# Kernel optimization log

Hardware: AMD Instinct MI355X
Metric: run time of the kernel (lower is better)

The kernel has to match this reference:

```python
import jax, jax.numpy as jnp
import numpy as np

RADIUS = 1.5
NUM_BASES = 128
HIDDEN = 256
B = 512        # molecules
N_ATOMS = 64   # atoms per molecule
BOX = 4.0      # box side -> density 1 atom/unit^3, avg degree ~8 at r=1.5
V = B * N_ATOMS
E_FIXED = 262144


def setup_inputs() -> dict:
    key = jax.random.key(0)
    kp, kx, kw1, kw2 = jax.random.split(key, 4)
    # positions, grouped per molecule so the radius graph respects batch_index
    pos = np.asarray(jax.random.uniform(kp, (B, N_ATOMS, 3), dtype=jnp.float32)) * BOX
    diff = pos[:, :, None, :] - pos[:, None, :, :]          # [B, n, n, 3]
    d2 = (diff ** 2).sum(-1)                                 # [B, n, n]
    mask = (d2 < RADIUS ** 2) & (~np.eye(N_ATOMS, dtype=bool)[None])
    b, i, j = np.nonzero(mask)
    src_all = (b * N_ATOMS + j).astype(np.int64)
    dest_all = (b * N_ATOMS + i).astype(np.int64)
    sel = np.resize(np.arange(len(src_all)), E_FIXED)        # fixed edge count for jit
    src = jnp.asarray(src_all[sel])
    dest = jnp.asarray(dest_all[sel])
    X = jax.random.normal(kx, (V, HIDDEN), dtype=jnp.float32)
    R = jnp.asarray(pos.reshape(V, 3))
    mu = jnp.linspace(0.0, RADIUS ** 2, NUM_BASES, dtype=jnp.float32)  # RBF centers over squared distance
    W1 = 0.05 * jax.random.normal(kw1, (NUM_BASES, HIDDEN), dtype=jnp.float32)
    W2 = 0.05 * jax.random.normal(kw2, (HIDDEN, HIDDEN), dtype=jnp.float32)
    batch_index = jnp.repeat(jnp.arange(B, dtype=jnp.int64), N_ATOMS)
    return {"X": X, "R": R, "W1": W1, "W2": W2, "mu": mu,
            "src": src, "dest": dest, "batch_index": batch_index}


def reference(X, R, W1, W2, mu, src, dest, batch_index):
    # batch_index only determines the (precomputed) radius graph; edges are src/dest.
    n_nodes = X.shape[0]
    D_ij = ((R[src] - R[dest]) ** 2).sum(-1)                 # [E] squared distance
    gamma = 1.0 / (mu[1] - mu[0]) ** 2
    rbf = jnp.exp(-gamma * (D_ij[:, None] - mu[None, :]) ** 2)  # [E, num_bases]
    h = jax.nn.relu(rbf @ W1)                                # [E, hidden]
    M_ij = jax.nn.relu(h @ W2)                               # [E, hidden] continuous filter
    msg = X[src] * M_ij                                      # [E, hidden]
    H = jax.ops.segment_sum(msg, dest, num_segments=n_nodes) # scatter-sum to nodes
    return H
```

## Files before the change

### kernel.cpp

```cpp
#include <hip/hip_runtime.h>
#include <hip/hip_bf16.h>

#define HIDDEN 256
#define NB 128
#define TB 32
#define E_TOTAL 262144
#define V_TOTAL 32768
#define R2MAX 2.25f

typedef __attribute__((ext_vector_type(8))) __bf16 bf16x8;
typedef __attribute__((ext_vector_type(4))) float floatx4;

__device__ inline unsigned short f2bf(float f) {
    union { float f; unsigned u; } v; v.f = f;
    unsigned r = v.u + 0x7fffu + ((v.u >> 16) & 1u);
    return (unsigned short)(r >> 16);
}

__global__ __launch_bounds__(512, 2)
void cfconv_build(const float* __restrict__ W1,
                  const float* __restrict__ W2,
                  const float* __restrict__ mu,
                  const float* __restrict__ X,
                  const int* __restrict__ dest,
                  unsigned short* __restrict__ tab16,
                  uint2* __restrict__ Xb,
                  int* __restrict__ cnt,
                  int* __restrict__ runstart,
                  float invScale, int nTabBlocks) {
    __shared__ __align__(16) float mulds[NB];
    __shared__ __align__(16) unsigned short h_lds[TB * HIDDEN];

    const int t = threadIdx.x;

    if (blockIdx.x >= nTabBlocks) {
        int rid = (blockIdx.x - nTabBlocks) * 512 + t;
        int rstride = (gridDim.x - nTabBlocks) * 512;
        for (int e = rid; e < E_TOTAL; e += rstride) {
            int d = dest[e];
            int dp = (e > 0) ? dest[e - 1] : -1;
            if (d != dp) {
                int k = atomicAdd(&cnt[d], 1);
                if (k < 2) runstart[2 * d + k] = e;
            }
        }
        int total = V_TOTAL * 64;
        for (int i = rid; i < total; i += rstride) {
            int v = i >> 6, s = i & 63;
            const float* xr = X + (size_t)v * HIDDEN + s;
            unsigned u0 = f2bf(xr[0]);
            unsigned u1 = f2bf(xr[64]);
            unsigned u2 = f2bf(xr[128]);
            unsigned u3 = f2bf(xr[192]);
            uint2 wv; wv.x = u0 | (u1 << 16); wv.y = u2 | (u3 << 16);
            Xb[i] = wv;
        }
        return;
    }

    const int eb = blockIdx.x * TB;

    if (t < NB) mulds[t] = mu[t];
    __syncthreads();

    const int lane = t & 63;
    const int w = t >> 6;
    const int wr = w >> 2;
    const int wc = w & 3;
    const int lhi = lane >> 4;
    const int llo = lane & 15;

    {
        float dm = mulds[1] - mulds[0];
        float ng = -1.0f / (dm * dm);
        float D0 = (float)(eb + 16 * wr + llo) * invScale;

        floatx4 acc[4];
        #pragma unroll
        for (int n = 0; n < 4; ++n) acc[n] = (floatx4)(0.0f);

        #pragma unroll
        for (int kc = 0; kc < 4; ++kc) {
            floatx4 mu0 = *(const floatx4*)(mulds + kc * 32 + lhi * 8);
            floatx4 mu1 = *(const floatx4*)(mulds + kc * 32 + lhi * 8 + 4);
            bf16x8 a, b[4];
            #pragma unroll
            for (int j = 0; j < 8; ++j) {
                float mv = (j < 4) ? mu0[j] : mu1[j - 4];
                float d = D0 - mv;
                a[j] = (__bf16)__expf(ng * d * d);
            }
            #pragma unroll
            for (int n = 0; n < 4; ++n) {
                const float* wb = W1 + (size_t)(kc * 32 + lhi * 8) * HIDDEN
                                     + wc * 64 + 16 * n + llo;
                #pragma unroll
                for (int j = 0; j < 8; ++j)
                    b[n][j] = (__bf16)wb[j * HIDDEN];
            }
            #pragma unroll
            for (int n = 0; n < 4; ++n)
                acc[n] = __builtin_amdgcn_mfma_f32_16x16x32_bf16(a, b[n], acc[n], 0, 0, 0);
        }

        char* hb = (char*)h_lds;
        #pragma unroll
        for (int n = 0; n < 4; ++n) {
            int col = wc * 64 + 16 * n + llo;
            #pragma unroll
            for (int r = 0; r < 4; ++r) {
                int row = 16 * wr + 4 * lhi + r;
                float v = fmaxf(acc[n][r], 0.0f);
                int byteoff = row * (HIDDEN * 2) + ((col * 2) ^ ((row & 7) << 4));
                *(__bf16*)(hb + byteoff) = (__bf16)v;
            }
        }
    }
    __syncthreads();

    floatx4 acc[4];
    {
        #pragma unroll
        for (int n = 0; n < 4; ++n) acc[n] = (floatx4)(0.0f);

        const char* hb = (const char*)h_lds;
        const int arow = 16 * wr + llo;
        #pragma unroll
        for (int kc = 0; kc < 8; ++kc) {
            bf16x8 a = *(const bf16x8*)(hb + arow * (HIDDEN * 2)
                          + ((kc * 64 + 16 * lhi) ^ ((arow & 7) << 4)));
            bf16x8 b[4];
            #pragma unroll
            for (int n = 0; n < 4; ++n) {
                const float* wb = W2 + (size_t)(kc * 32 + lhi * 8) * HIDDEN
                                     + wc * 64 + 16 * n + llo;
                #pragma unroll
                for (int j = 0; j < 8; ++j)
                    b[n][j] = (__bf16)wb[j * HIDDEN];
            }
            #pragma unroll
            for (int n = 0; n < 4; ++n)
                acc[n] = __builtin_amdgcn_mfma_f32_16x16x32_bf16(a, b[n], acc[n], 0, 0, 0);
        }
    }
    __syncthreads();

    {
        char* hb = (char*)h_lds;
        #pragma unroll
        for (int n = 0; n < 4; ++n) {
            int col = wc * 64 + 16 * n + llo;
            #pragma unroll
            for (int r = 0; r < 4; ++r) {
                int row = 16 * wr + 4 * lhi + r;
                float v = fmaxf(acc[n][r], 0.0f);
                int byteoff = row * (HIDDEN * 2) + ((col * 2) ^ ((row & 7) << 4));
                *(__bf16*)(hb + byteoff) = (__bf16)v;
            }
        }
    }
    __syncthreads();

    {
        const char* hb = (const char*)h_lds;
        const int s = t & 63;
        const int rg = t >> 6;
        #pragma unroll
        for (int rr = 0; rr < 4; ++rr) {
            int row = rg * 4 + rr;
            int sw = (row & 7) << 4;
            unsigned u0 = *(const unsigned short*)(hb + row * 512 + ((2 * s) ^ sw));
            unsigned u1 = *(const unsigned short*)(hb + row * 512 + ((2 * (s + 64)) ^ sw));
            unsigned u2 = *(const unsigned short*)(hb + row * 512 + ((2 * (s + 128)) ^ sw));
            unsigned u3 = *(const unsigned short*)(hb + row * 512 + ((2 * (s + 192)) ^ sw));
            uint2 wv; wv.x = u0 | (u1 << 16); wv.y = u2 | (u3 << 16);
            *(uint2*)((char*)tab16 + (size_t)(eb + row) * 512 + s * 8) = wv;
        }
    }
}

__global__ __launch_bounds__(512)
void cfconv_gather(const uint2* __restrict__ Xb,
                   const float* __restrict__ R,
                   const char* __restrict__ tab,
                   const int* __restrict__ src,
                   const int* __restrict__ dest,
                   const int* __restrict__ cnt,
                   const int* __restrict__ runstart,
                   float* __restrict__ out,
                   float scale, int Tm1) {
    __shared__ __align__(16) uint2 xs[64 * 64];
    __shared__ __align__(16) float4 rs4[64];

    const int t = threadIdx.x;
    const int orig = blockIdx.x;
    const int cpx = gridDim.x >> 3;
    const int wg = (orig & 7) * cpx + (orig >> 3);
    const int mol = wg >> 1;
    const int half = wg & 1;
    const int vbase = mol * 64;

    {
        const uint2* slab = Xb + (size_t)vbase * 64;
        #pragma unroll
        for (int k = 0; k < 8; ++k)
            xs[k * 512 + t] = slab[k * 512 + t];
        if (t < 64) {
            const float* rp = R + (size_t)(vbase + t) * 3;
            rs4[t] = make_float4(rp[0], rp[1], rp[2], 0.0f);
        }
    }
    __syncthreads();

    const int lane = t & 63;
    const int w = t >> 6;

#define ACC8(qt, qx) { \
    union { unsigned u; float f; } mm_, xx_; \
    mm_.u = (qt).x << 16;          xx_.u = (qx).x << 16;          a0 = fmaf(mm_.f, xx_.f, a0); \
    mm_.u = (qt).x & 0xffff0000u;  xx_.u = (qx).x & 0xffff0000u;  a1 = fmaf(mm_.f, xx_.f, a1); \
    mm_.u = (qt).y << 16;          xx_.u = (qx).y << 16;          a2 = fmaf(mm_.f, xx_.f, a2); \
    mm_.u = (qt).y & 0xffff0000u;  xx_.u = (qx).y & 0xffff0000u;  a3 = fmaf(mm_.f, xx_.f, a3); }

    for (int nn = 0; nn < 4; ++nn) {
        const int vloc = (half << 5) + (w << 2) + nn;
        const int v = vbase + vloc;

        float a0 = 0.f, a1 = 0.f, a2 = 0.f, a3 = 0.f;

        int nr = cnt[v];
        if (nr > 0) {
            nr = min(nr, 2);
            int r0 = runstart[2 * v];
            int r1 = (nr == 2) ? runstart[2 * v + 1] : 0;
            int sA = (nr == 2) ? min(r0, r1) : r0;
            int sB = (nr == 2) ? max(r0, r1) : 0;

            const float4 rv = rs4[vloc];
            const char* tabc = tab + lane * 8;

            for (int run = 0; run < nr; ++run) {
                int s = (run == 0) ? sA : sB;
                const int limit = (run == 0 && nr == 2) ? sB : E_TOTAL;
                int len;
                do {
                    int e = s + lane;
                    int ec = min(e, E_TOTAL - 1);
                    int d = dest[ec];
                    int si = src[ec];
                    bool valid = (e < limit) && (d == v);
                    int sil = (si - vbase) & 63;
                    float4 rsrc = rs4[sil];
                    float dx = rsrc.x - rv.x;
                    float dy = rsrc.y - rv.y;
                    float dz = rsrc.z - rv.z;
                    float D = dx * dx + dy * dy + dz * dz;
                    int i0 = min((int)(D * scale + 0.5f), Tm1);
                    int io = i0 << 9;
                    unsigned long long mask = __ballot(valid);
                    len = (~mask == 0ull) ? 64 : __builtin_ctzll(~mask);

                    for (int base = 0; base < len; base += 8) {
#define CH(j) \
    int ioj_##j = __builtin_amdgcn_readlane(io, min(base + j, len - 1)); \
    int sil_##j = __builtin_amdgcn_readlane(sil, min(base + j, len - 1)); \
    uint2 qt_##j = *(const uint2*)(tabc + ioj_##j); \
    uint2 qx_##j = xs[(sil_##j << 6) + lane];
                        CH(0) CH(1) CH(2) CH(3) CH(4) CH(5) CH(6) CH(7)
#undef CH
                        ACC8(qt_0, qx_0)
                        if (base + 1 < len) ACC8(qt_1, qx_1)
                        if (base + 2 < len) ACC8(qt_2, qx_2)
                        if (base + 3 < len) ACC8(qt_3, qx_3)
                        if (base + 4 < len) ACC8(qt_4, qx_4)
                        if (base + 5 < len) ACC8(qt_5, qx_5)
                        if (base + 6 < len) ACC8(qt_6, qx_6)
                        if (base + 7 < len) ACC8(qt_7, qx_7)
                    }
                    s += len;
                } while (len == 64);
            }
        }

        float* orow = out + (size_t)v * HIDDEN + lane;
        orow[0]   = a0;
        orow[64]  = a1;
        orow[128] = a2;
        orow[192] = a3;
    }
#undef ACC8
}

extern "C" void kernel_launch(void* const* d_in, const int* in_sizes, int n_in,
                              void* d_out, int out_size, void* d_ws, size_t ws_size,
                              hipStream_t stream) {
    const float* X  = (const float*)d_in[0];
    const float* R  = (const float*)d_in[1];
    const float* W1 = (const float*)d_in[2];
    const float* W2 = (const float*)d_in[3];
    const float* mu = (const float*)d_in[4];
    const int* src  = (const int*)d_in[5];
    const int* dest = (const int*)d_in[6];
    float* out = (float*)d_out;

    int T = 4096;
    const size_t xb_bytes = (size_t)V_TOTAL * HIDDEN * 2;
    const size_t aux_bytes = (size_t)V_TOTAL * 4 * 3;
    if (ws_size > 0) {
        while (T > 64 && (size_t)T * HIDDEN * 2 + xb_bytes + aux_bytes > ws_size) T >>= 1;
    }
    unsigned short* tab = (unsigned short*)d_ws;
    uint2* Xb = (uint2*)((char*)d_ws + (size_t)T * HIDDEN * 2);
    int* cnt = (int*)((char*)Xb + xb_bytes);
    int* runstart = cnt + V_TOTAL;

    const float scale = (float)(T - 1) / R2MAX;
    const float invScale = R2MAX / (float)(T - 1);

    int nTabBlocks = T / TB;
    int riderBlocks = 512;

    hipMemsetAsync(cnt, 0, V_TOTAL * sizeof(int), stream);

    cfconv_build<<<nTabBlocks + riderBlocks, 512, 0, stream>>>(
        W1, W2, mu, X, dest, tab, Xb, cnt, runstart, invScale, nTabBlocks);

    cfconv_gather<<<V_TOTAL / 32, 512, 0, stream>>>(
        Xb, R, (const char*)tab, src, dest, cnt, runstart, out, scale, T - 1);
}
```

Baseline: 48.45 us.

## Fuse X-to-bf16 conversion into gather kernel and vectorize per-wave run metadata loads

Drops the separate pass in the build kernel that converts X to a bf16 workspace copy. The gather kernel now reads fp32 X directly and packs it into shared memory itself, removing one full write and read of the intermediate array. Per-node run counts and starts are now loaded once per wave as int4 vectors. Rider blocks drop from 512 to 128. The trade-off is that the gather kernel reads twice the bytes of X, and each molecule's X is converted twice because two workgroups share a molecule.

```diff
diff --git a/kernel.cpp b/kernel.cpp
--- a/kernel.cpp
+++ b/kernel.cpp
@@ -21,10 +21,8 @@
 void cfconv_build(const float* __restrict__ W1,
                   const float* __restrict__ W2,
                   const float* __restrict__ mu,
-                  const float* __restrict__ X,
                   const int* __restrict__ dest,
                   unsigned short* __restrict__ tab16,
-                  uint2* __restrict__ Xb,
                   int* __restrict__ cnt,
                   int* __restrict__ runstart,
                   float invScale, int nTabBlocks) {
@@ -44,17 +42,6 @@
                 if (k < 2) runstart[2 * d + k] = e;
             }
         }
-        int total = V_TOTAL * 64;
-        for (int i = rid; i < total; i += rstride) {
-            int v = i >> 6, s = i & 63;
-            const float* xr = X + (size_t)v * HIDDEN + s;
-            unsigned u0 = f2bf(xr[0]);
-            unsigned u1 = f2bf(xr[64]);
-            unsigned u2 = f2bf(xr[128]);
-            unsigned u3 = f2bf(xr[192]);
-            uint2 wv; wv.x = u0 | (u1 << 16); wv.y = u2 | (u3 << 16);
-            Xb[i] = wv;
-        }
         return;
     }
 
@@ -180,7 +167,7 @@
 }
 
 __global__ __launch_bounds__(512)
-void cfconv_gather(const uint2* __restrict__ Xb,
+void cfconv_gather(const float* __restrict__ X,
                    const float* __restrict__ R,
                    const char* __restrict__ tab,
                    const int* __restrict__ src,
@@ -200,20 +187,27 @@
     const int half = wg & 1;
     const int vbase = mol * 64;
 
-    {
-        const uint2* slab = Xb + (size_t)vbase * 64;
-        #pragma unroll
-        for (int k = 0; k < 8; ++k)
-            xs[k * 512 + t] = slab[k * 512 + t];
+    const int lane = t & 63;
+    const int wv8 = t >> 6;
+
+    {
+        #pragma unroll
+        for (int k = 0; k < 8; ++k) {
+            int row = wv8 * 8 + k;
+            const float* xr = X + (size_t)(vbase + row) * HIDDEN + lane;
+            unsigned u0 = f2bf(xr[0]);
+            unsigned u1 = f2bf(xr[64]);
+            unsigned u2 = f2bf(xr[128]);
+            unsigned u3 = f2bf(xr[192]);
+            uint2 wv; wv.x = u0 | (u1 << 16); wv.y = u2 | (u3 << 16);
+            xs[(row << 6) + lane] = wv;
+        }
         if (t < 64) {
             const float* rp = R + (size_t)(vbase + t) * 3;
             rs4[t] = make_float4(rp[0], rp[1], rp[2], 0.0f);
         }
     }
     __syncthreads();
-
-    const int lane = t & 63;
-    const int w = t >> 6;
 
 #define ACC8(qt, qx) { \
     union { unsigned u; float f; } mm_, xx_; \
@@ -222,17 +216,26 @@
     mm_.u = (qt).y << 16;          xx_.u = (qx).y << 16;          a2 = fmaf(mm_.f, xx_.f, a2); \
     mm_.u = (qt).y & 0xffff0000u;  xx_.u = (qx).y & 0xffff0000u;  a3 = fmaf(mm_.f, xx_.f, a3); }
 
+    const int vwave = vbase + (half << 5) + (wv8 << 2);
+    int4 c4 = *(const int4*)(cnt + vwave);
+    int4 ra = *(const int4*)(runstart + 2 * vwave);
+    int4 rb = *(const int4*)(runstart + 2 * vwave + 4);
+    int cnta[4] = {c4.x, c4.y, c4.z, c4.w};
+    int run0[4] = {ra.x, ra.z, rb.x, rb.z};
+    int run1[4] = {ra.y, ra.w, rb.y, rb.w};
+
+    #pragma unroll
     for (int nn = 0; nn < 4; ++nn) {
-        const int vloc = (half << 5) + (w << 2) + nn;
+        const int vloc = (half << 5) + (wv8 << 2) + nn;
         const int v = vbase + vloc;
 
         float a0 = 0.f, a1 = 0.f, a2 = 0.f, a3 = 0.f;
 
-        int nr = cnt[v];
+        int nr = cnta[nn];
         if (nr > 0) {
             nr = min(nr, 2);
-            int r0 = runstart[2 * v];
-            int r1 = (nr == 2) ? runstart[2 * v + 1] : 0;
+            int r0 = run0[nn];
+            int r1 = (nr == 2) ? run1[nn] : 0;
             int sA = (nr == 2) ? min(r0, r1) : r0;
             int sB = (nr == 2) ? max(r0, r1) : 0;
 
@@ -304,27 +307,25 @@
     float* out = (float*)d_out;
 
     int T = 4096;
-    const size_t xb_bytes = (size_t)V_TOTAL * HIDDEN * 2;
     const size_t aux_bytes = (size_t)V_TOTAL * 4 * 3;
     if (ws_size > 0) {
-        while (T > 64 && (size_t)T * HIDDEN * 2 + xb_bytes + aux_bytes > ws_size) T >>= 1;
+        while (T > 64 && (size_t)T * HIDDEN * 2 + aux_bytes > ws_size) T >>= 1;
     }
     unsigned short* tab = (unsigned short*)d_ws;
-    uint2* Xb = (uint2*)((char*)d_ws + (size_t)T * HIDDEN * 2);
-    int* cnt = (int*)((char*)Xb + xb_bytes);
+    int* cnt = (int*)((char*)d_ws + (size_t)T * HIDDEN * 2);
     int* runstart = cnt + V_TOTAL;
 
     const float scale = (float)(T - 1) / R2MAX;
     const float invScale = R2MAX / (float)(T - 1);
 
     int nTabBlocks = T / TB;
-    int riderBlocks = 512;
+    int riderBlocks = 128;
 
     hipMemsetAsync(cnt, 0, V_TOTAL * sizeof(int), stream);
 
     cfconv_build<<<nTabBlocks + riderBlocks, 512, 0, stream>>>(
-        W1, W2, mu, X, dest, tab, Xb, cnt, runstart, invScale, nTabBlocks);
+        W1, W2, mu, dest, tab, cnt, runstart, invScale, nTabBlocks);
 
     cfconv_gather<<<V_TOTAL / 32, 512, 0, stream>>>(
-        Xb, R, (const char*)tab, src, dest, cnt, runstart, out, scale, T - 1);
+        X, R, (const char*)tab, src, dest, cnt, runstart, out, scale, T - 1);
 }
```

Result: slower. 52.98 us (+9.4%).

## Batch per-node metadata loads and interleave two nodes' gather-accumulate loops

Applied to the files above, without the earlier changes.

Each wave now loads the run counts and run starts for all four of its nodes with vector loads, then computes the edge metadata (table offset, source slot, run length) for all four nodes before doing any accumulation. The accumulation then walks two nodes at once, issuing the LDS and table loads of both before their FMAs, with 16 accumulators held in registers. The aim is to hide the latency of the dependent global loads and LDS gathers that the old one-node-at-a-time loop serialised. In exchange, register pressure goes up and the loop over a run is dropped, so each run is assumed to fit in one 64-lane window (true while each molecule has 64 atoms).

```diff
diff --git a/kernel.cpp b/kernel.cpp
--- a/kernel.cpp
+++ b/kernel.cpp
@@ -213,82 +213,142 @@
     __syncthreads();
 
     const int lane = t & 63;
-    const int w = t >> 6;
-
-#define ACC8(qt, qx) { \
+    const int wv8 = t >> 6;
+    const int vloc0 = (half << 5) + (wv8 << 2);
+
+    const int vwave = vbase + vloc0;
+    int4 c4 = *(const int4*)(cnt + vwave);
+    int4 ra = *(const int4*)(runstart + 2 * vwave);
+    int4 rb = *(const int4*)(runstart + 2 * vwave + 4);
+    int cnta[4] = {c4.x, c4.y, c4.z, c4.w};
+    int run0[4] = {ra.x, ra.z, rb.x, rb.z};
+    int run1[4] = {ra.y, ra.w, rb.y, rb.w};
+
+    int sAv[4], limv[4], dmv[4], smv[4];
+    #pragma unroll
+    for (int nn = 0; nn < 4; ++nn) {
+        int nr = cnta[nn];
+        int r0 = run0[nn], r1 = run1[nn];
+        int sA = r0, lim = E_TOTAL;
+        if (nr >= 2) { sA = min(r0, r1); lim = max(r0, r1); }
+        if (nr <= 0) { sA = 0; lim = 0; }
+        sAv[nn] = sA; limv[nn] = lim;
+        int ec = min(sA + lane, E_TOTAL - 1);
+        dmv[nn] = dest[ec];
+        smv[nn] = src[ec];
+    }
+
+    const char* tabc = tab + lane * 8;
+
+    int io0_, io1_, io2_, io3_;
+    int sl0_, sl1_, sl2_, sl3_;
+    int ln0_, ln1_, ln2_, ln3_;
+#define META(nn, IO, SL, LN) { \
+    int v_ = vwave + nn; \
+    int e_ = sAv[nn] + lane; \
+    bool valid_ = (e_ < limv[nn]) && (dmv[nn] == v_); \
+    int sil_ = (smv[nn] - vbase) & 63; \
+    float4 rs_ = rs4[sil_]; \
+    float4 rv_ = rs4[vloc0 + nn]; \
+    float dx_ = rs_.x - rv_.x, dy_ = rs_.y - rv_.y, dz_ = rs_.z - rv_.z; \
+    float D_ = dx_ * dx_ + dy_ * dy_ + dz_ * dz_; \
+    int i0_ = min((int)(D_ * scale + 0.5f), Tm1); \
+    IO = i0_ << 9; SL = sil_; \
+    unsigned long long m_ = __ballot(valid_); \
+    LN = (~m_ == 0ull) ? 64 : __builtin_ctzll(~m_); }
+    META(0, io0_, sl0_, ln0_)
+    META(1, io1_, sl1_, ln1_)
+    META(2, io2_, sl2_, ln2_)
+    META(3, io3_, sl3_, ln3_)
+#undef META
+
+#define ACC8e(qt, qx, c0, c1, c2, c3) { \
     union { unsigned u; float f; } mm_, xx_; \
-    mm_.u = (qt).x << 16;          xx_.u = (qx).x << 16;          a0 = fmaf(mm_.f, xx_.f, a0); \
-    mm_.u = (qt).x & 0xffff0000u;  xx_.u = (qx).x & 0xffff0000u;  a1 = fmaf(mm_.f, xx_.f, a1); \
-    mm_.u = (qt).y << 16;          xx_.u = (qx).y << 16;          a2 = fmaf(mm_.f, xx_.f, a2); \
-    mm_.u = (qt).y & 0xffff0000u;  xx_.u = (qx).y & 0xffff0000u;  a3 = fmaf(mm_.f, xx_.f, a3); }
-
-    for (int nn = 0; nn < 4; ++nn) {
-        const int vloc = (half << 5) + (w << 2) + nn;
-        const int v = vbase + vloc;
-
-        float a0 = 0.f, a1 = 0.f, a2 = 0.f, a3 = 0.f;
-
-        int nr = cnt[v];
-        if (nr > 0) {
-            nr = min(nr, 2);
-            int r0 = runstart[2 * v];
-            int r1 = (nr == 2) ? runstart[2 * v + 1] : 0;
-            int sA = (nr == 2) ? min(r0, r1) : r0;
-            int sB = (nr == 2) ? max(r0, r1) : 0;
-
-            const float4 rv = rs4[vloc];
-            const char* tabc = tab + lane * 8;
-
-            for (int run = 0; run < nr; ++run) {
-                int s = (run == 0) ? sA : sB;
-                const int limit = (run == 0 && nr == 2) ? sB : E_TOTAL;
-                int len;
-                do {
-                    int e = s + lane;
-                    int ec = min(e, E_TOTAL - 1);
-                    int d = dest[ec];
-                    int si = src[ec];
-                    bool valid = (e < limit) && (d == v);
-                    int sil = (si - vbase) & 63;
-                    float4 rsrc = rs4[sil];
-                    float dx = rsrc.x - rv.x;
-                    float dy = rsrc.y - rv.y;
-                    float dz = rsrc.z - rv.z;
-                    float D = dx * dx + dy * dy + dz * dz;
-                    int i0 = min((int)(D * scale + 0.5f), Tm1);
-                    int io = i0 << 9;
-                    unsigned long long mask = __ballot(valid);
-                    len = (~mask == 0ull) ? 64 : __builtin_ctzll(~mask);
-
-                    for (int base = 0; base < len; base += 8) {
-#define CH(j) \
-    int ioj_##j = __builtin_amdgcn_readlane(io, min(base + j, len - 1)); \
-    int sil_##j = __builtin_amdgcn_readlane(sil, min(base + j, len - 1)); \
-    uint2 qt_##j = *(const uint2*)(tabc + ioj_##j); \
-    uint2 qx_##j = xs[(sil_##j << 6) + lane];
-                        CH(0) CH(1) CH(2) CH(3) CH(4) CH(5) CH(6) CH(7)
-#undef CH
-                        ACC8(qt_0, qx_0)
-                        if (base + 1 < len) ACC8(qt_1, qx_1)
-                        if (base + 2 < len) ACC8(qt_2, qx_2)
-                        if (base + 3 < len) ACC8(qt_3, qx_3)
-                        if (base + 4 < len) ACC8(qt_4, qx_4)
-                        if (base + 5 < len) ACC8(qt_5, qx_5)
-                        if (base + 6 < len) ACC8(qt_6, qx_6)
-                        if (base + 7 < len) ACC8(qt_7, qx_7)
-                    }
-                    s += len;
-                } while (len == 64);
-            }
-        }
-
-        float* orow = out + (size_t)v * HIDDEN + lane;
-        orow[0]   = a0;
-        orow[64]  = a1;
-        orow[128] = a2;
-        orow[192] = a3;
-    }
-#undef ACC8
+    mm_.u = (qt).x << 16;          xx_.u = (qx).x << 16;          c0 = fmaf(mm_.f, xx_.f, c0); \
+    mm_.u = (qt).x & 0xffff0000u;  xx_.u = (qx).x & 0xffff0000u;  c1 = fmaf(mm_.f, xx_.f, c1); \
+    mm_.u = (qt).y << 16;          xx_.u = (qx).y << 16;          c2 = fmaf(mm_.f, xx_.f, c2); \
+    mm_.u = (qt).y & 0xffff0000u;  xx_.u = (qx).y & 0xffff0000u;  c3 = fmaf(mm_.f, xx_.f, c3); }
+
+#define LD4(P, IO, SL, B) \
+    int P##iA = __builtin_amdgcn_readlane((IO), ((B) + 0) & 63); \
+    int P##sA = __builtin_amdgcn_readlane((SL), ((B) + 0) & 63); \
+    int P##iB = __builtin_amdgcn_readlane((IO), ((B) + 1) & 63); \
+    int P##sB = __builtin_amdgcn_readlane((SL), ((B) + 1) & 63); \
+    int P##iC = __builtin_amdgcn_readlane((IO), ((B) + 2) & 63); \
+    int P##sC = __builtin_amdgcn_readlane((SL), ((B) + 2) & 63); \
+    int P##iD = __builtin_amdgcn_readlane((IO), ((B) + 3) & 63); \
+    int P##sD = __builtin_amdgcn_readlane((SL), ((B) + 3) & 63); \
+    uint2 P##tA = *(const uint2*)(tabc + P##iA); uint2 P##xA = xs[(P##sA << 6) + lane]; \
+    uint2 P##tB = *(const uint2*)(tabc + P##iB); uint2 P##xB = xs[(P##sB << 6) + lane]; \
+    uint2 P##tC = *(const uint2*)(tabc + P##iC); uint2 P##xC = xs[(P##sC << 6) + lane]; \
+    uint2 P##tD = *(const uint2*)(tabc + P##iD); uint2 P##xD = xs[(P##sD << 6) + lane];
+
+#define ACC4(P, LN, B, c0, c1, c2, c3) \
+    if ((B) + 0 < (LN)) ACC8e(P##tA, P##xA, c0, c1, c2, c3) \
+    if ((B) + 1 < (LN)) ACC8e(P##tB, P##xB, c0, c1, c2, c3) \
+    if ((B) + 2 < (LN)) ACC8e(P##tC, P##xC, c0, c1, c2, c3) \
+    if ((B) + 3 < (LN)) ACC8e(P##tD, P##xD, c0, c1, c2, c3)
+
+#define PAIR(IOA, SLA, LNA, IOB, SLB, LNB, p0, p1, p2, p3, q0, q1, q2, q3) { \
+    int lmax_ = (LNA) > (LNB) ? (LNA) : (LNB); \
+    for (int base_ = 0; base_ < lmax_; base_ += 4) { \
+        LD4(PA_, IOA, SLA, base_) \
+        LD4(PB_, IOB, SLB, base_) \
+        ACC4(PA_, LNA, base_, p0, p1, p2, p3) \
+        ACC4(PB_, LNB, base_, q0, q1, q2, q3) \
+    } }
+
+#define RUN2(nn, c0, c1, c2, c3) \
+    if (cnta[nn] >= 2) { \
+        int v_ = vwave + nn; \
+        int s2_ = max(run0[nn], run1[nn]); \
+        int e_ = s2_ + lane; \
+        int ec_ = min(e_, E_TOTAL - 1); \
+        int d_ = dest[ec_]; \
+        int si_ = src[ec_]; \
+        bool valid_ = (e_ < E_TOTAL) && (d_ == v_); \
+        int sil_ = (si_ - vbase) & 63; \
+        float4 rs_ = rs4[sil_]; \
+        float4 rv_ = rs4[vloc0 + nn]; \
+        float dx_ = rs_.x - rv_.x, dy_ = rs_.y - rv_.y, dz_ = rs_.z - rv_.z; \
+        float D_ = dx_ * dx_ + dy_ * dy_ + dz_ * dz_; \
+        int i0_ = min((int)(D_ * scale + 0.5f), Tm1); \
+        int iow_ = i0_ << 9; \
+        unsigned long long m_ = __ballot(valid_); \
+        int lnw_ = (~m_ == 0ull) ? 64 : __builtin_ctzll(~m_); \
+        for (int base_ = 0; base_ < lnw_; base_ += 4) { \
+            LD4(PC_, iow_, sil_, base_) \
+            ACC4(PC_, lnw_, base_, c0, c1, c2, c3) \
+        } \
+    }
+
+    float a00 = 0.f, a01 = 0.f, a02 = 0.f, a03 = 0.f;
+    float a10 = 0.f, a11 = 0.f, a12 = 0.f, a13 = 0.f;
+    float a20 = 0.f, a21 = 0.f, a22 = 0.f, a23 = 0.f;
+    float a30 = 0.f, a31 = 0.f, a32 = 0.f, a33 = 0.f;
+
+    PAIR(io0_, sl0_, ln0_, io1_, sl1_, ln1_, a00, a01, a02, a03, a10, a11, a12, a13)
+    PAIR(io2_, sl2_, ln2_, io3_, sl3_, ln3_, a20, a21, a22, a23, a30, a31, a32, a33)
+
+    RUN2(0, a00, a01, a02, a03)
+    RUN2(1, a10, a11, a12, a13)
+    RUN2(2, a20, a21, a22, a23)
+    RUN2(3, a30, a31, a32, a33)
+
+#define STOREROW(nn, c0, c1, c2, c3) { \
+    float* orow_ = out + (size_t)(vwave + nn) * HIDDEN + lane; \
+    orow_[0] = c0; orow_[64] = c1; orow_[128] = c2; orow_[192] = c3; }
+    STOREROW(0, a00, a01, a02, a03)
+    STOREROW(1, a10, a11, a12, a13)
+    STOREROW(2, a20, a21, a22, a23)
+    STOREROW(3, a30, a31, a32, a33)
+
+#undef ACC8e
+#undef LD4
+#undef ACC4
+#undef PAIR
+#undef RUN2
+#undef STOREROW
 }
 
 extern "C" void kernel_launch(void* const* d_in, const int* in_sizes, int n_in,
```

Measured after the change: 50.24 us. +3.7%, slower.
